# Kernel tuning notes

Measured on AMD Instinct MI355X. Metric: run time of the kernel, lower is better.

Reference implementation:

```python
import jax, jax.numpy as jnp
import numpy as np


def _hadamard(n: int) -> np.ndarray:
    # Sylvester construction; n must be a power of 2 (asserted in the torch source).
    H = np.array([[1.0]], dtype=np.float32)
    while H.shape[0] < n:
        H = np.block([[H, H], [H, -H]])
    return (H * (n ** -0.5)).astype(np.float32)


def _rotate_activation(x):
    # hadamard_transform(x, scale=D**-0.5) over the last dim; bf16 in/out like the CUDA kernel.
    D = x.shape[-1]
    H = jnp.asarray(_hadamard(D))
    return (x.astype(jnp.float32) @ H).astype(x.dtype)


def _cu_seqlen_kv_bounds(seq_lens, num_ctx_tokens):
    # Vectorized equivalent of compute_cu_seqlen_kv_bounds_nocache (repeat_interleave -> searchsorted).
    offsets = jnp.concatenate([jnp.zeros(1, jnp.int32), jnp.cumsum(seq_lens).astype(jnp.int32)])
    pos = jnp.arange(num_ctx_tokens, dtype=jnp.int32)
    batch_ids = jnp.searchsorted(offsets, pos, side='right').astype(jnp.int32) - 1
    ks = offsets[batch_ids]                 # start of this token's sequence in packed KV
    ke = ks + (pos - ks) + 1                # causal: local_position + 1 past the start
    return ks, ke


def setup_inputs() -> dict:
    key = jax.random.key(0)
    k1, k2, k3 = jax.random.split(key, 3)
    T, H, D = 2048, 16, 128
    q = jax.random.normal(k1, (T, H, D), dtype=jnp.bfloat16)
    k = jax.random.normal(k2, (T, D), dtype=jnp.bfloat16)
    weights = jax.random.uniform(k3, (T, H), dtype=jnp.float32) * (H ** -0.5)
    seq_lens = jnp.array([1024, 1024], dtype=jnp.int32)
    return {"q": q, "k": k, "weights": weights, "seq_lens": seq_lens, "index_topk": 256}


def reference(q, k, weights, seq_lens, index_topk):
    T = q.shape[0]
    # Hadamard-rotate q and k (lightning indexer activation rotation).
    qr = _rotate_activation(q).astype(jnp.float32)   # [T, H, D]
    kr = _rotate_activation(k).astype(jnp.float32)   # [T, D]
    # Index score: I[t, s] = sum_h w[t, h] * relu(q[t, h] . k[s])
    logits = jnp.einsum('thd,sd->ths', qr, kr)       # [T, H, T]
    scores = jnp.einsum('ths,th->ts', jax.nn.relu(logits), weights)  # [T, T]
    # Causal ragged-batch KV window per token.
    ks, ke = _cu_seqlen_kv_bounds(seq_lens, T)
    pos = jnp.arange(T, dtype=jnp.int32)
    valid = (pos[None, :] >= ks[:, None]) & (pos[None, :] < ke[:, None])
    NEG = jnp.float32(-1e30)
    masked = jnp.where(valid, scores, NEG)
    topk_vals, topk_idx = jax.lax.top_k(masked, index_topk)  # [T, topk]
    return topk_vals, topk_idx
```

## Files before the change

kernel.cpp:

```cpp
#include <hip/hip_runtime.h>
#include <hip/hip_bf16.h>
#include <stdint.h>

typedef __attribute__((ext_vector_type(8))) short short8;
typedef __attribute__((ext_vector_type(4))) float float4_t;
typedef __attribute__((ext_vector_type(16))) float float16_t;

#define DDIM 128
#define SORTN 256
#define LROW 136
#define SCAP 1088
#define NCHT 17

__device__ inline unsigned short f32_to_bf16_rne(float f) {
    uint32_t u = __float_as_uint(f);
    return (unsigned short)((u + 0x7FFFu + ((u >> 16) & 1u)) >> 16);
}
__device__ inline float bf16_to_f32(unsigned short h) {
    return __uint_as_float(((uint32_t)h) << 16);
}
__device__ inline int ks_of(const int* seq_lens, int n_seq, int t) {
    int off = 0, r = 0;
    for (int i = 0; i < n_seq; ++i) {
        int nx = off + seq_lens[i];
        if (t < nx) { r = off; break; }
        off = nx;
    }
    return r;
}

__global__ __launch_bounds__(256) void rotate_k_kernel(
        const unsigned short* __restrict__ k, unsigned short* __restrict__ kr, int T) {
    int row = blockIdx.x * 16 + (threadIdx.x >> 4);
    if (row >= T) return;
    int l16 = threadIdx.x & 15;
    short8 in = *(const short8*)(k + (size_t)row * DDIM + 8 * l16);
    float f[8];
    #pragma unroll
    for (int j = 0; j < 8; ++j) f[j] = bf16_to_f32((unsigned short)in[j]);
    #pragma unroll
    for (int b = 1; b <= 4; b <<= 1)
        #pragma unroll
        for (int j = 0; j < 8; ++j)
            if (!(j & b)) { float a = f[j], c = f[j | b]; f[j] = a + c; f[j | b] = a - c; }
    #pragma unroll
    for (int m = 1; m <= 8; m <<= 1) {
        bool hi = (l16 & m) != 0;
        #pragma unroll
        for (int j = 0; j < 8; ++j) {
            float o = __shfl_xor(f[j], m, 64);
            f[j] = hi ? (o - f[j]) : (f[j] + o);
        }
    }
    const float sc = 0.08838834764831845f;
    short8 out;
    #pragma unroll
    for (int j = 0; j < 8; ++j) out[j] = (short)f32_to_bf16_rne(f[j] * sc);
    *(short8*)(kr + (size_t)row * DDIM + 8 * l16) = out;
}

__global__ __launch_bounds__(256, 2) void fused_kernel(
        const unsigned short* __restrict__ q,
        const unsigned short* __restrict__ kr,
        const float* __restrict__ w,
        const int* __restrict__ seq_lens, int n_seq,
        float* __restrict__ out_vals, float* __restrict__ out_idx,
        int T, int H, int K, int Tt) {
    __shared__ __align__(16) float scw[4][SCAP];
    unsigned short* qst = (unsigned short*)&scw[0][0];

    const int tid  = threadIdx.x;
    const int wv   = tid >> 6, lane = tid & 63;
    const int col  = lane & 15, kgrp = lane >> 4;
    const int hi   = lane >> 5;
    const int l31  = lane & 31;

    const int m     = blockIdx.x;
    const int halfG = Tt >> 1;
    const int ttile = (Tt <= 1) ? 0 : ((m < halfG) ? m : (Tt - 1 - (m - halfG)));
    const int tt0   = ttile * 4;

    const int tg1 = tt0 + 1, tg2 = tt0 + 2, tg3 = tt0 + 3;
    const bool v0 = (tt0 < T), v1 = (tg1 < T), v2 = (tg2 < T), v3 = (tg3 < T);
    const int t0 = v0 ? tt0 : T - 1, t1 = v1 ? tg1 : T - 1;
    const int t2 = v2 ? tg2 : T - 1, t3 = v3 ? tg3 : T - 1;
    const int ks0 = ks_of(seq_lens, n_seq, t0);
    const int ks1 = ks_of(seq_lens, n_seq, t1);
    const int ks2 = ks_of(seq_lens, n_seq, t2);
    const int ks3 = ks_of(seq_lens, n_seq, t3);

    const int bks    = ks_of(seq_lens, n_seq, tt0);
    const int bke    = (tt0 + 4 < T) ? (tt0 + 4) : T;
    const int nchunk = (bke - bks + 127) >> 7;

    const int nrow = wv * 32 + l31;

    auto load_chunk = [&](short8* dst, int kv0) {
        int gr = kv0 + nrow; if (gr > T - 1) gr = T - 1;
        const unsigned short* base = kr + (size_t)gr * DDIM + hi * 8;
        #pragma unroll
        for (int k8 = 0; k8 < 8; ++k8) dst[k8] = *(const short8*)(base + 16 * k8);
    };

    short8 bA[8], bB[8];
    load_chunk(bA, bks);

    const int t_r = (tt0 + wv < T) ? (tt0 + wv) : (T - 1);
    float f[4][8];
    const unsigned short* qrow = q + ((size_t)t_r * H + col) * DDIM + kgrp * 8;
    #pragma unroll
    for (int kk = 0; kk < 4; ++kk) {
        short8 v = *(const short8*)(qrow + kk * 32);
        #pragma unroll
        for (int j = 0; j < 8; ++j) f[kk][j] = bf16_to_f32((unsigned short)v[j]);
    }
    #pragma unroll
    for (int b = 1; b <= 4; b <<= 1)
        #pragma unroll
        for (int kk = 0; kk < 4; ++kk)
            #pragma unroll
            for (int j = 0; j < 8; ++j)
                if (!(j & b)) { float a = f[kk][j], c = f[kk][j | b];
                                f[kk][j] = a + c; f[kk][j | b] = a - c; }
    #pragma unroll
    for (int kk = 0; kk < 4; ++kk)
        #pragma unroll
        for (int j = 0; j < 8; ++j) {
            float o = __shfl_xor(f[kk][j], 16, 64);
            f[kk][j] = (kgrp & 1) ? (o - f[kk][j]) : (f[kk][j] + o);
        }
    #pragma unroll
    for (int kk = 0; kk < 4; ++kk)
        #pragma unroll
        for (int j = 0; j < 8; ++j) {
            float o = __shfl_xor(f[kk][j], 32, 64);
            f[kk][j] = (kgrp & 2) ? (o - f[kk][j]) : (f[kk][j] + o);
        }
    #pragma unroll
    for (int j = 0; j < 8; ++j) {
        { float a = f[0][j], c = f[1][j]; f[0][j] = a + c; f[1][j] = a - c; }
        { float a = f[2][j], c = f[3][j]; f[2][j] = a + c; f[3][j] = a - c; }
        { float a = f[0][j], c = f[2][j]; f[0][j] = a + c; f[2][j] = a - c; }
        { float a = f[1][j], c = f[3][j]; f[1][j] = a + c; f[3][j] = a - c; }
    }
    const float scl = 0.08838834764831845f;
    #pragma unroll
    for (int kk = 0; kk < 4; ++kk) {
        short8 o;
        #pragma unroll
        for (int j = 0; j < 8; ++j) o[j] = (short)f32_to_bf16_rne(f[kk][j] * scl);
        *(short8*)&qst[(wv * 16 + col) * LROW + kgrp * 8 + kk * 32] = o;
    }
    __syncthreads();

    short8 afrag0[8], afrag1[8];
    {
        const unsigned short* qr0 = qst + l31 * LROW + hi * 8;
        const unsigned short* qr1 = qst + (32 + l31) * LROW + hi * 8;
        #pragma unroll
        for (int k8 = 0; k8 < 8; ++k8) {
            afrag0[k8] = *(const short8*)(qr0 + 16 * k8);
            afrag1[k8] = *(const short8*)(qr1 + 16 * k8);
        }
    }
    float w0r[8], w1r[8], w2r[8], w3r[8];
    #pragma unroll
    for (int r = 0; r < 8; ++r) {
        int h = (r & 3) + 8 * ((r >> 2) & 1) + 4 * hi;
        w0r[r] = w[(size_t)t0 * H + h];
        w1r[r] = w[(size_t)t1 * H + h];
        w2r[r] = w[(size_t)t2 * H + h];
        w3r[r] = w[(size_t)t3 * H + h];
    }
    __syncthreads();

    auto compute_chunk = [&](const short8* bf, int kv0) {
        float16_t acc01 = {0.f, 0.f, 0.f, 0.f, 0.f, 0.f, 0.f, 0.f,
                           0.f, 0.f, 0.f, 0.f, 0.f, 0.f, 0.f, 0.f};
        float16_t acc23 = {0.f, 0.f, 0.f, 0.f, 0.f, 0.f, 0.f, 0.f,
                           0.f, 0.f, 0.f, 0.f, 0.f, 0.f, 0.f, 0.f};
        __builtin_amdgcn_s_setprio(1);
        #pragma unroll
        for (int k8 = 0; k8 < 8; ++k8) {
            acc01 = __builtin_amdgcn_mfma_f32_32x32x16_bf16(afrag0[k8], bf[k8], acc01, 0, 0, 0);
            acc23 = __builtin_amdgcn_mfma_f32_32x32x16_bf16(afrag1[k8], bf[k8], acc23, 0, 0, 0);
        }
        __builtin_amdgcn_s_setprio(0);
        float p0 = 0.f, p1 = 0.f, p2 = 0.f, p3 = 0.f;
        #pragma unroll
        for (int r = 0; r < 8; ++r) {
            float a = acc01[r];     a = a > 0.f ? a : 0.f; p0 += w0r[r] * a;
            float b = acc01[r + 8]; b = b > 0.f ? b : 0.f; p1 += w1r[r] * b;
            float g = acc23[r];     g = g > 0.f ? g : 0.f; p2 += w2r[r] * g;
            float d = acc23[r + 8]; d = d > 0.f ? d : 0.f; p3 += w3r[r] * d;
        }
        p0 += __shfl_xor(p0, 32, 64);
        p1 += __shfl_xor(p1, 32, 64);
        p2 += __shfl_xor(p2, 32, 64);
        p3 += __shfl_xor(p3, 32, 64);
        const int s = kv0 + nrow;
        if (hi == 0) {
            if (v0 && s >= ks0 && s <= t0) scw[0][s - ks0] = p0;
            if (v2 && s >= ks2 && s <= t2) scw[2][s - ks2] = p2;
        } else {
            if (v1 && s >= ks1 && s <= t1) scw[1][s - ks1] = p1;
            if (v3 && s >= ks3 && s <= t3) scw[3][s - ks3] = p3;
        }
    };

    for (int c = 0; c < nchunk; c += 2) {
        if (c + 1 < nchunk) load_chunk(bB, bks + ((c + 1) << 7));
        compute_chunk(bA, bks + (c << 7));
        if (c + 1 < nchunk) {
            if (c + 2 < nchunk) load_chunk(bA, bks + ((c + 2) << 7));
            compute_chunk(bB, bks + ((c + 1) << 7));
        }
    }
    __syncthreads();

    const int t_s = tt0 + wv;
    if (t_s >= T) return;
    const int ks_w = ks_of(seq_lens, n_seq, t_s);
    const int ke_w = t_s + 1;
    const int n    = ke_w - ks_w;

    const int nch = (n + 63) >> 6;
    uint32_t ukey[NCHT];
    #pragma unroll
    for (int c = 0; c < NCHT; ++c) {
        if (c < nch) {
            int i = c * 64 + lane;
            ukey[c] = (i < n) ? __float_as_uint(scw[wv][i]) : 0u;
        } else ukey[c] = 0u;
    }
    unsigned long long* candw = (unsigned long long*)&scw[wv][0];

    const int Keff = (n < K) ? n : K;
    uint32_t ustar = 0;
    int ttake = K;
    if (n > K) {
        uint32_t lo = 0, hia = 0x80000000u;
        for (int it = 0; it < 31; ++it) {
            uint32_t mid = (lo + hia) >> 1;
            int total = 0;
            #pragma unroll
            for (int c = 0; c < NCHT; ++c)
                if (c < nch) total += (int)__popcll(__ballot(ukey[c] >= mid));
            if (total >= K) lo = mid; else hia = mid;
        }
        ustar = lo;
        int tg = 0;
        #pragma unroll
        for (int c = 0; c < NCHT; ++c)
            if (c < nch) tg += (int)__popcll(__ballot(ukey[c] > ustar));
        ttake = K - tg;
    }

    {
        const unsigned long long ltm = (1ull << lane) - 1ull;
        int base = 0, tieBase = 0;
        const bool selAll = (n <= K);
        #pragma unroll
        for (int c = 0; c < NCHT; ++c) {
            if (c < nch) {
                int i = c * 64 + lane;
                bool inb = (i < n);
                uint32_t u = ukey[c];
                bool isGt  = inb && (selAll || u > ustar);
                bool isTie = inb && !selAll && (u == ustar);
                unsigned long long mt = __ballot(isTie);
                int tr = tieBase + (int)__popcll(mt & ltm);
                bool take = isGt || (isTie && tr < ttake);
                unsigned long long mk = __ballot(take);
                if (take) {
                    int pos = base + (int)__popcll(mk & ltm);
                    int s = ks_w + i;
                    if (pos < SORTN)
                        candw[pos] = ((((unsigned long long)u << 11) |
                                       (unsigned long long)(T - 1 - s)) + 1ull);
                }
                base    += (int)__popcll(mk);
                tieBase += (int)__popcll(mt);
            }
        }
        for (int i = Keff + lane; i < SORTN; i += 64) candw[i] = 0ull;
    }

    unsigned long long kreg[4];
    #pragma unroll
    for (int r = 0; r < 4; ++r) kreg[r] = candw[4 * lane + r];

    #define CX(a, b, dsc) { unsigned long long _mx = (a) > (b) ? (a) : (b); \
                            unsigned long long _mn = (a) > (b) ? (b) : (a); \
                            (a) = (dsc) ? _mx : _mn; (b) = (dsc) ? _mn : _mx; }
    #pragma unroll
    for (int size = 2; size <= SORTN; size <<= 1) {
        #pragma unroll
        for (int stride = SORTN >> 1; stride >= 4; stride >>= 1) {
            if (stride > (size >> 1)) continue;
            int lmask = stride >> 2;
            #pragma unroll
            for (int r = 0; r < 4; ++r) {
                int e = 4 * lane + r;
                unsigned long long other = __shfl_xor(kreg[r], lmask, 64);
                bool desc = ((e & size) == 0);
                bool iAmLow = ((e & stride) == 0);
                bool keepMax = (iAmLow == desc);
                kreg[r] = keepMax ? (kreg[r] > other ? kreg[r] : other)
                                  : (kreg[r] < other ? kreg[r] : other);
            }
        }
        if (size >= 4) {
            bool d = (((4 * lane) & size) == 0);
            CX(kreg[0], kreg[2], d);
            CX(kreg[1], kreg[3], d);
            CX(kreg[0], kreg[1], d);
            CX(kreg[2], kreg[3], d);
        } else {
            CX(kreg[0], kreg[1], true);
            CX(kreg[2], kreg[3], false);
        }
    }
    #undef CX

    if (4 * lane < K) {
        float4_t v4, i4;
        #pragma unroll
        for (int r = 0; r < 4; ++r) {
            int e = 4 * lane + r;
            unsigned long long key = kreg[r];
            float v; int idx;
            if (key != 0ull) {
                unsigned long long km1 = key - 1ull;
                v = __uint_as_float((uint32_t)(km1 >> 11));
                idx = T - 1 - (int)(km1 & 0x7FFull);
            } else {
                int pidx = e - Keff;
                idx = (pidx < ks_w) ? pidx : (ke_w + (pidx - ks_w));
                v = -1e30f;
            }
            v4[r] = v; i4[r] = (float)idx;
        }
        *(float4_t*)(out_vals + (size_t)t_s * K + 4 * lane) = v4;
        *(float4_t*)(out_idx  + (size_t)t_s * K + 4 * lane) = i4;
    }
}

extern "C" void kernel_launch(void* const* d_in, const int* in_sizes, int n_in,
                              void* d_out, int out_size, void* d_ws, size_t ws_size,
                              hipStream_t stream) {
    const unsigned short* q = (const unsigned short*)d_in[0];
    const unsigned short* k = (const unsigned short*)d_in[1];
    const float* w          = (const float*)d_in[2];
    const int* seq_lens     = (const int*)d_in[3];
    const int n_seq = in_sizes[3];
    const int T = in_sizes[1] / DDIM;
    const int H = in_sizes[2] / T;
    const int K = out_size / (2 * T);

    unsigned short* kr = (unsigned short*)d_ws;
    float* out_vals = (float*)d_out;
    float* out_idx  = out_vals + (size_t)T * K;

    rotate_k_kernel<<<dim3((T + 15) / 16), dim3(256), 0, stream>>>(k, kr, T);
    const int Tt = (T + 3) / 4;
    fused_kernel<<<dim3(Tt), dim3(256), 0, stream>>>(
        q, kr, w, seq_lens, n_seq, out_vals, out_idx, T, H, K, Tt);
}
```

Before: 102.8 us.

## Write rotated K in MFMA-fragment-tiled layout for coalesced chunk loads

The K-rotation kernel now also writes a second copy of rotated K, padded by 128 rows, in a tiled layout. Each lane of a wave can then fetch its MFMA B-fragment with fully contiguous 16-byte loads. The fused kernel uses this layout when the sequence start is 32-aligned and otherwise falls back to the strided row-major loads. This aims to cut the scattered global-load cost in the main loop, at the price of extra workspace, extra writes in the rotate kernel, and a runtime branch.

```diff
diff --git a/kernel.cpp b/kernel.cpp
--- a/kernel.cpp
+++ b/kernel.cpp
@@ -30,11 +30,13 @@
 }
 
 __global__ __launch_bounds__(256) void rotate_k_kernel(
-        const unsigned short* __restrict__ k, unsigned short* __restrict__ kr, int T) {
+        const unsigned short* __restrict__ k, unsigned short* __restrict__ kr,
+        unsigned short* __restrict__ kr2, int T, int Tpad) {
     int row = blockIdx.x * 16 + (threadIdx.x >> 4);
-    if (row >= T) return;
+    if (row >= Tpad) return;
+    int rs = (row < T) ? row : (T - 1);
     int l16 = threadIdx.x & 15;
-    short8 in = *(const short8*)(k + (size_t)row * DDIM + 8 * l16);
+    short8 in = *(const short8*)(k + (size_t)rs * DDIM + 8 * l16);
     float f[8];
     #pragma unroll
     for (int j = 0; j < 8; ++j) f[j] = bf16_to_f32((unsigned short)in[j]);
@@ -56,12 +58,17 @@
     short8 out;
     #pragma unroll
     for (int j = 0; j < 8; ++j) out[j] = (short)f32_to_bf16_rne(f[j] * sc);
-    *(short8*)(kr + (size_t)row * DDIM + 8 * l16) = out;
+    if (row < T)
+        *(short8*)(kr + (size_t)row * DDIM + 8 * l16) = out;
+    const size_t slot = (size_t)(row >> 5) * 512 + (size_t)(l16 >> 1) * 64
+                      + (size_t)(l16 & 1) * 32 + (row & 31);
+    *(short8*)(kr2 + (slot << 3)) = out;
 }
 
 __global__ __launch_bounds__(256, 2) void fused_kernel(
         const unsigned short* __restrict__ q,
         const unsigned short* __restrict__ kr,
+        const unsigned short* __restrict__ kr2,
         const float* __restrict__ w,
         const int* __restrict__ seq_lens, int n_seq,
         float* __restrict__ out_vals, float* __restrict__ out_idx,
@@ -92,14 +99,25 @@
     const int bks    = ks_of(seq_lens, n_seq, tt0);
     const int bke    = (tt0 + 4 < T) ? (tt0 + 4) : T;
     const int nchunk = (bke - bks + 127) >> 7;
+    const bool aligned = ((bks & 31) == 0);
 
     const int nrow = wv * 32 + l31;
 
-    auto load_chunk = [&](short8* dst, int kv0) {
+    auto load_fast = [&](short8* dst, int kv0) {
+        const size_t B = (size_t)((kv0 >> 5) + wv);
+        const unsigned short* base = kr2 + ((B * 512 + lane) << 3);
+        #pragma unroll
+        for (int k8 = 0; k8 < 8; ++k8)
+            dst[k8] = *(const short8*)(base + ((size_t)k8 << 12));
+    };
+    auto load_slow = [&](short8* dst, int kv0) {
         int gr = kv0 + nrow; if (gr > T - 1) gr = T - 1;
         const unsigned short* base = kr + (size_t)gr * DDIM + hi * 8;
         #pragma unroll
         for (int k8 = 0; k8 < 8; ++k8) dst[k8] = *(const short8*)(base + 16 * k8);
+    };
+    auto load_chunk = [&](short8* dst, int kv0) {
+        if (aligned) load_fast(dst, kv0); else load_slow(dst, kv0);
     };
 
     short8 bA[8], bB[8];
@@ -357,13 +375,16 @@
     const int T = in_sizes[1] / DDIM;
     const int H = in_sizes[2] / T;
     const int K = out_size / (2 * T);
-
-    unsigned short* kr = (unsigned short*)d_ws;
+    const int Tpad = T + 128;
+
+    unsigned short* kr  = (unsigned short*)d_ws;
+    unsigned short* kr2 = kr + (size_t)T * DDIM;
     float* out_vals = (float*)d_out;
     float* out_idx  = out_vals + (size_t)T * K;
 
-    rotate_k_kernel<<<dim3((T + 15) / 16), dim3(256), 0, stream>>>(k, kr, T);
+    rotate_k_kernel<<<dim3((Tpad + 15) / 16), dim3(256), 0, stream>>>(
+        k, kr, kr2, T, Tpad);
     const int Tt = (T + 3) / 4;
     fused_kernel<<<dim3(Tt), dim3(256), 0, stream>>>(
-        q, kr, w, seq_lens, n_seq, out_vals, out_idx, T, H, K, Tt);
-}
+        q, kr, kr2, w, seq_lens, n_seq, out_vals, out_idx, T, H, K, Tt);
+}
```

New measurement: 103.8 us. Within noise of the previous version (+1.0%).
